# Kernel optimization log

Hardware: AMD Instinct MI355X
Metric: run time of the kernel (lower is better)

The kernel has to match this reference:

```python
import jax, jax.numpy as jnp
import numpy as np

NEG_SLOPE = 0.2  # PyG GATConv default negative_slope


def _gat_conv(x, src, dst, W, a_src, a_dst, bias, heads, concat):
    """PyG-style GATConv (eval mode, self-loops already appended to src/dst).
    x: [N, Fin], W: [Fin, heads*C], a_src/a_dst: [heads, C], bias matches output.
    """
    N = x.shape[0]
    C = W.shape[1] // heads
    xw = (x @ W).reshape(N, heads, C)                      # [N, H, C]
    alpha_s = jnp.sum(xw * a_src, axis=-1)                 # [N, H]
    alpha_d = jnp.sum(xw * a_dst, axis=-1)                 # [N, H]
    e = jax.nn.leaky_relu(alpha_s[src] + alpha_d[dst], NEG_SLOPE)  # [E, H]
    # softmax over incoming edges of each destination node (numerically stable)
    m = jax.ops.segment_max(e, dst, num_segments=N)        # [N, H]
    e = jnp.exp(e - m[dst])
    denom = jax.ops.segment_sum(e, dst, num_segments=N)    # [N, H]
    alpha = e / denom[dst]                                 # [E, H]
    out = jax.ops.segment_sum(alpha[:, :, None] * xw[src], dst, num_segments=N)  # [N, H, C]
    if concat:
        out = out.reshape(N, heads * C)
    else:
        out = out.mean(axis=1)
    return out + bias


def setup_inputs() -> dict:
    key = jax.random.key(0)
    ks = jax.random.split(key, 10)
    N, E, FIN, FOUT, H1, C1 = 100000, 1600000, 128, 16, 4, 8
    x = jax.random.normal(ks[0], (N, FIN), jnp.float32)
    edge_index = jax.random.randint(ks[1], (2, E), 0, N, dtype=jnp.int32)
    W1 = jax.random.normal(ks[2], (FIN, H1 * C1), jnp.float32) / np.sqrt(FIN)
    a1_src = jax.random.normal(ks[3], (H1, C1), jnp.float32) / np.sqrt(C1)
    a1_dst = jax.random.normal(ks[4], (H1, C1), jnp.float32) / np.sqrt(C1)
    b1 = jnp.zeros((H1 * C1,), jnp.float32)
    W2 = jax.random.normal(ks[5], (H1 * C1, FOUT), jnp.float32) / np.sqrt(H1 * C1)
    a2_src = jax.random.normal(ks[6], (1, FOUT), jnp.float32) / np.sqrt(FOUT)
    a2_dst = jax.random.normal(ks[7], (1, FOUT), jnp.float32) / np.sqrt(FOUT)
    b2 = jnp.zeros((FOUT,), jnp.float32)
    return {"x": x, "edge_index": edge_index, "W1": W1, "a1_src": a1_src,
            "a1_dst": a1_dst, "b1": b1, "W2": W2, "a2_src": a2_src,
            "a2_dst": a2_dst, "b2": b2}


def reference(x, edge_index, W1, a1_src, a1_dst, b1, W2, a2_src, a2_dst, b2):
    N = x.shape[0]
    # PyG GATConv add_self_loops=True default
    loop = jnp.arange(N, dtype=edge_index.dtype)
    src = jnp.concatenate([edge_index[0], loop])
    dst = jnp.concatenate([edge_index[1], loop])
    # eval mode: F.dropout is identity
    h = _gat_conv(x, src, dst, W1, a1_src, a1_dst, b1, heads=4, concat=True)
    h = jax.nn.elu(h)
    h = _gat_conv(h, src, dst, W2, a2_src, a2_dst, b2, heads=1, concat=True)
    return jax.nn.log_softmax(h, axis=1)
```

## Files before the change

### kernel.cpp

```cpp
#include <hip/hip_runtime.h>
#include <math.h>

#define NN 100000
#define NE 1600000
#define ET (NE + NN)
#define FIN 128
#define H1 4
#define C1 8
#define F1 32
#define FOUT 16
#define NSLOPE 0.2f

#define PARTW 256
#define PSHIFT 8
#define NPART ((NN + PARTW - 1) / PARTW)
#define CHUNK 8192
#define NBLK ((ET + CHUNK - 1) / CHUNK)
#define CPAD 16
#define SMASK 0x1FFFF

typedef _Float16 half8 __attribute__((ext_vector_type(8)));
typedef _Float16 half4_t __attribute__((ext_vector_type(4)));
typedef _Float16 half2_t __attribute__((ext_vector_type(2)));
typedef float f32x4 __attribute__((ext_vector_type(4)));

template <int SEL>
__device__ inline float fp8dec(unsigned int w) {
    return __builtin_amdgcn_cvt_f32_fp8((int)w, SEL);
}


__device__ inline int wave_incl_scan(int v) {
#pragma unroll
    for (int off = 1; off < 64; off <<= 1) {
        int u = __shfl_up(v, off);
        if ((threadIdx.x & 63) >= off) v += u;
    }
    return v;
}

__device__ inline int block_excl_scan(int v, int* wsum, int nw) {
    int t = threadIdx.x, wid = t >> 6, lane = t & 63;
    int incl = wave_incl_scan(v);
    if (lane == 63) wsum[wid] = incl;
    __syncthreads();
    if (wid == 0) {
        int wv = (lane < nw) ? wsum[lane] : 0;
        wv = wave_incl_scan(wv);
        if (lane < nw) wsum[lane] = wv;
    }
    __syncthreads();
    return incl - v + (wid ? wsum[wid - 1] : 0);
}


__global__ __launch_bounds__(1024) void k_hist(const int* __restrict__ dstA, int* __restrict__ ptotal) {
    __shared__ int h[NPART];
    int t = threadIdx.x;
    for (int i = t; i < NPART; i += 1024) h[i] = 0;
    __syncthreads();
    int base = blockIdx.x * CHUNK;
#pragma unroll
    for (int k = 0; k < CHUNK / 1024; k++) {
        int e = base + k * 1024 + t;
        if (e < ET) {
            int d = (e < NE) ? dstA[e] : (e - NE);
            atomicAdd(&h[d >> PSHIFT], 1);
        }
    }
    __syncthreads();
    for (int i = t; i < NPART; i += 1024)
        if (h[i]) atomicAdd(&ptotal[i * CPAD], h[i]);
}

__global__ __launch_bounds__(512) void k_pbase(const int* __restrict__ ptotal, int* __restrict__ pbase,
                                               int* __restrict__ gcur, int* __restrict__ rowstart) {
    __shared__ int wsum[8];
    int t = threadIdx.x;
    int v = (t < NPART) ? ptotal[t * CPAD] : 0;
    int excl = block_excl_scan(v, wsum, 8);
    if (t < NPART) { pbase[t] = excl; gcur[t * CPAD] = excl; }
    if (t == 0) { pbase[NPART] = ET; rowstart[NN] = ET; }
}

__global__ __launch_bounds__(1024) void k_part(const int* __restrict__ srcA, const int* __restrict__ dstA,
                                               int* __restrict__ gcur, int* __restrict__ pairs) {
    __shared__ int h[NPART];
    __shared__ int cur[NPART];
    int t = threadIdx.x;
    for (int i = t; i < NPART; i += 1024) h[i] = 0;
    __syncthreads();
    int base = blockIdx.x * CHUNK;
#pragma unroll
    for (int k = 0; k < CHUNK / 1024; k++) {
        int e = base + k * 1024 + t;
        if (e < ET) {
            int d = (e < NE) ? dstA[e] : (e - NE);
            atomicAdd(&h[d >> PSHIFT], 1);
        }
    }
    __syncthreads();
    for (int i = t; i < NPART; i += 1024) {
        int c = h[i];
        cur[i] = c ? atomicAdd(&gcur[i * CPAD], c) : 0;
    }
    __syncthreads();
#pragma unroll
    for (int k = 0; k < CHUNK / 1024; k++) {
        int e = base + k * 1024 + t;
        if (e < ET) {
            int s, d;
            if (e < NE) { s = srcA[e]; d = dstA[e]; }
            else        { s = e - NE;  d = s; }
            int pos = atomicAdd(&cur[d >> PSHIFT], 1);
            pairs[pos] = ((d & (PARTW - 1)) << 17) | s;
        }
    }
}

__global__ __launch_bounds__(1024) void k_sort(const int* __restrict__ pbase, const int* __restrict__ pairs,
                                               int* __restrict__ rowstart, int* __restrict__ epack) {
    __shared__ int hist[PARTW];
    __shared__ int sa[PARTW], sb[PARTW];
    int p = blockIdx.x;
    int t = threadIdx.x;
    int n0 = p << PSHIFT;
    int nn = min(PARTW, NN - n0);
    int base = pbase[p];
    int cnt = pbase[p + 1] - base;
    if (t < PARTW) hist[t] = 0;
    __syncthreads();
    for (int i = t; i < cnt; i += 1024)
        atomicAdd(&hist[pairs[base + i] >> 17], 1);
    __syncthreads();
    if (t < PARTW) sa[t] = hist[t];
    __syncthreads();
    int* pin = sa; int* pout = sb;
    for (int off = 1; off < PARTW; off <<= 1) {
        if (t < PARTW) pout[t] = pin[t] + ((t >= off) ? pin[t - off] : 0);
        __syncthreads();
        int* tmp = pin; pin = pout; pout = tmp;
    }
    int excl = 0;
    if (t < PARTW) {
        excl = pin[t] - hist[t];
        if (t < nn) rowstart[n0 + t] = base + excl;
    }
    __syncthreads();
    if (t < PARTW) hist[t] = excl;
    __syncthreads();
    for (int i = t; i < cnt; i += 1024) {
        int v = pairs[base + i];
        int pos = base + atomicAdd(&hist[v >> 17], 1);
        epack[pos] = v;
    }
}


__global__ __launch_bounds__(256) void k_gemm1(const float* __restrict__ x, const float* __restrict__ W1,
        const float* __restrict__ a1s, const float* __restrict__ a1d,
        unsigned int* __restrict__ xc1, float* __restrict__ ad1) {
    __shared__ _Float16 w1t[F1 * FIN];
    __shared__ float xs[256 * F1];
    int t = threadIdx.x;
    {
        int i0 = t * 16;
#pragma unroll
        for (int i = 0; i < 16; i++) {
            int idx = i0 + i;
            int k = idx >> 5, n = idx & 31;
            w1t[n * FIN + k] = (_Float16)W1[idx];
        }
    }
    __syncthreads();
    int w = t >> 6, l = t & 63;
    int q = l >> 4, r16 = l & 15;
    int nblk = blockIdx.x * 256;
    int n0 = nblk + w * 64;
    half8 bf[4][2];
#pragma unroll
    for (int kc = 0; kc < 4; kc++)
#pragma unroll
        for (int nt = 0; nt < 2; nt++)
            bf[kc][nt] = *(const half8*)&w1t[(nt * 16 + r16) * FIN + kc * 32 + q * 8];
#pragma unroll
    for (int mt = 0; mt < 4; mt++) {
        int row = n0 + mt * 16 + r16;
        int rowc = min(row, NN - 1);
        const float4* xp = (const float4*)(x + (size_t)rowc * FIN + q * 8);
        half8 af[4];
#pragma unroll
        for (int kc = 0; kc < 4; kc++) {
            float4 u = xp[kc * 8];
            float4 v = xp[kc * 8 + 1];
            half8 a;
            a[0] = (_Float16)u.x; a[1] = (_Float16)u.y; a[2] = (_Float16)u.z; a[3] = (_Float16)u.w;
            a[4] = (_Float16)v.x; a[5] = (_Float16)v.y; a[6] = (_Float16)v.z; a[7] = (_Float16)v.w;
            af[kc] = a;
        }
        f32x4 acc0 = {0.f, 0.f, 0.f, 0.f};
        f32x4 acc1 = {0.f, 0.f, 0.f, 0.f};
#pragma unroll
        for (int kc = 0; kc < 4; kc++) {
            acc0 = __builtin_amdgcn_mfma_f32_16x16x32_f16(af[kc], bf[kc][0], acc0, 0, 0, 0);
            acc1 = __builtin_amdgcn_mfma_f32_16x16x32_f16(af[kc], bf[kc][1], acc1, 0, 0, 0);
        }
#pragma unroll
        for (int r = 0; r < 4; r++) {
            xs[(w * 64 + mt * 16 + q * 4 + r) * F1 + r16] = acc0[r];
            xs[(w * 64 + mt * 16 + q * 4 + r) * F1 + 16 + r16] = acc1[r];
        }
    }
    int node = nblk + w * 64 + l;
    if (node < NN) {
        const float4* xr = (const float4*)&xs[(w * 64 + l) * F1];
        float rowv[F1];
#pragma unroll
        for (int j = 0; j < 8; j++) {
            float4 v = xr[j];
            rowv[j * 4] = v.x; rowv[j * 4 + 1] = v.y; rowv[j * 4 + 2] = v.z; rowv[j * 4 + 3] = v.w;
        }
        float ss[H1], dd[H1];
#pragma unroll
        for (int h = 0; h < H1; h++) {
            ss[h] = 0.f; dd[h] = 0.f;
#pragma unroll
            for (int c = 0; c < C1; c++) {
                ss[h] = fmaf(rowv[h * C1 + c], a1s[h * C1 + c], ss[h]);
                dd[h] = fmaf(rowv[h * C1 + c], a1d[h * C1 + c], dd[h]);
            }
        }
        uint4 o[4];
        unsigned int* ow = (unsigned int*)o;
#pragma unroll
        for (int c4 = 0; c4 < 8; c4++) {
            int p = 0;
            p = __builtin_amdgcn_cvt_pk_fp8_f32(rowv[c4 * 4 + 0], rowv[c4 * 4 + 1], p, false);
            p = __builtin_amdgcn_cvt_pk_fp8_f32(rowv[c4 * 4 + 2], rowv[c4 * 4 + 3], p, true);
            ow[2 * c4] = (unsigned int)p;
            ow[2 * c4 + 1] = __float_as_uint(ss[c4 >> 1]);
        }
        uint4* o16 = (uint4*)(xc1 + (size_t)node * 16);
        o16[0] = o[0];
        o16[1] = o[1];
        o16[2] = o[2];
        o16[3] = o[3];
        ((float4*)ad1)[node] = make_float4(dd[0], dd[1], dd[2], dd[3]);
    }
}


__global__ __launch_bounds__(256) void k_gather1(const int* __restrict__ rowstart, const int* __restrict__ epack,
        const float* __restrict__ ad1, const unsigned int* __restrict__ xc1,
        const float* __restrict__ b1, _Float16* __restrict__ h1h) {
    int n = blockIdx.x * 4 + (threadIdx.x >> 6);
    if (n >= NN) return;
    int l = threadIdx.x & 63;
    int g = l >> 3;
    int j = l & 7;
    int h = j >> 1;
    float adh = ad1[n * H1 + h];
    const uint2* xrow = (const uint2*)xc1;
    int beg = rowstart[n], end = rowstart[n + 1];
    float a0 = 0.f, a1 = 0.f, a2 = 0.f, a3 = 0.f, ad = 0.f;
    int i = beg + g;
    int c0 = epack[i] & SMASK, c1 = epack[i + 8] & SMASK;
    int sn0 = epack[i + 16] & SMASK, sn1 = epack[i + 24] & SMASK;
    uint2 t0 = xrow[c0 * 8 + j], t1 = xrow[c1 * 8 + j];
    unsigned int v0 = t0.x, v1 = t1.x;
    float f0 = __uint_as_float(t0.y), f1 = __uint_as_float(t1.y);
    while (i + 8 < end) {
        uint2 n0v = xrow[sn0 * 8 + j], n1v = xrow[sn1 * 8 + j];
        int u0 = epack[i + 32] & SMASK, u1 = epack[i + 40] & SMASK;
        float e0 = f0 + adh, e1 = f1 + adh;
        e0 = fmaxf(e0, NSLOPE * e0);
        e1 = fmaxf(e1, NSLOPE * e1);
        float w0 = __expf(e0), w1 = __expf(e1);
        ad += w0 + w1;
        a0 = fmaf(w0, fp8dec<0>(v0), fmaf(w1, fp8dec<0>(v1), a0));
        a1 = fmaf(w0, fp8dec<1>(v0), fmaf(w1, fp8dec<1>(v1), a1));
        a2 = fmaf(w0, fp8dec<2>(v0), fmaf(w1, fp8dec<2>(v1), a2));
        a3 = fmaf(w0, fp8dec<3>(v0), fmaf(w1, fp8dec<3>(v1), a3));
        v0 = n0v.x; v1 = n1v.x;
        f0 = __uint_as_float(n0v.y); f1 = __uint_as_float(n1v.y);
        sn0 = u0; sn1 = u1;
        i += 16;
    }
    if (i < end) {
        float e0 = f0 + adh;
        e0 = fmaxf(e0, NSLOPE * e0);
        float w0 = __expf(e0);
        ad += w0;
        a0 = fmaf(w0, fp8dec<0>(v0), a0);
        a1 = fmaf(w0, fp8dec<1>(v0), a1);
        a2 = fmaf(w0, fp8dec<2>(v0), a2);
        a3 = fmaf(w0, fp8dec<3>(v0), a3);
    }
#pragma unroll
    for (int off = 8; off < 64; off <<= 1) {
        a0 += __shfl_xor(a0, off);
        a1 += __shfl_xor(a1, off);
        a2 += __shfl_xor(a2, off);
        a3 += __shfl_xor(a3, off);
        ad += __shfl_xor(ad, off);
    }
    if (l < 8) {
        float inv = 1.0f / ad;
        float y0 = fmaf(a0, inv, b1[4 * j]);
        float y1 = fmaf(a1, inv, b1[4 * j + 1]);
        float y2 = fmaf(a2, inv, b1[4 * j + 2]);
        float y3 = fmaf(a3, inv, b1[4 * j + 3]);
        y0 = (y0 > 0.f) ? y0 : expm1f(y0);
        y1 = (y1 > 0.f) ? y1 : expm1f(y1);
        y2 = (y2 > 0.f) ? y2 : expm1f(y2);
        y3 = (y3 > 0.f) ? y3 : expm1f(y3);
        half4_t o;
        o[0] = (_Float16)y0; o[1] = (_Float16)y1; o[2] = (_Float16)y2; o[3] = (_Float16)y3;
        ((half4_t*)h1h)[(size_t)n * 8 + j] = o;
    }
}


__global__ __launch_bounds__(256) void k_node2(const _Float16* __restrict__ h1h, const float* __restrict__ W2,
        const float* __restrict__ a2s, const float* __restrict__ a2d,
        unsigned int* __restrict__ xc2, float* __restrict__ ad2) {
    int n = blockIdx.x * 256 + threadIdx.x;
    if (n >= NN) return;
    float acc[FOUT];
#pragma unroll
    for (int j = 0; j < FOUT; j++) acc[j] = 0.f;
    const half8* h8 = (const half8*)(h1h + (size_t)n * F1);
#pragma unroll
    for (int i8 = 0; i8 < F1 / 8; i8++) {
        half8 hv = h8[i8];
#pragma unroll
        for (int kk = 0; kk < 8; kk++) {
            float hk = (float)hv[kk];
            int i = i8 * 8 + kk;
#pragma unroll
            for (int j = 0; j < FOUT; j++)
                acc[j] = fmaf(hk, W2[i * FOUT + j], acc[j]);
        }
    }
    float ss = 0.f, dd = 0.f;
#pragma unroll
    for (int j = 0; j < FOUT; j++) {
        ss = fmaf(acc[j], a2s[j], ss);
        dd = fmaf(acc[j], a2d[j], dd);
    }
    uint4 o[4];
    unsigned int* ow = (unsigned int*)o;
    unsigned int ssu = __float_as_uint(ss);
#pragma unroll
    for (int p = 0; p < 8; p++) {
        half2_t hp;
        hp[0] = (_Float16)acc[2 * p];
        hp[1] = (_Float16)acc[2 * p + 1];
        ow[2 * p] = *(unsigned int*)&hp;
        ow[2 * p + 1] = ssu;
    }
    uint4* o16 = (uint4*)(xc2 + (size_t)n * 16);
    o16[0] = o[0];
    o16[1] = o[1];
    o16[2] = o[2];
    o16[3] = o[3];
    ad2[n] = dd;
}


__global__ __launch_bounds__(256) void k_gather2(const int* __restrict__ rowstart, const int* __restrict__ epack,
        const float* __restrict__ ad2, const unsigned int* __restrict__ xc2,
        const float* __restrict__ b2, float* __restrict__ out) {
    int n = blockIdx.x * 4 + (threadIdx.x >> 6);
    if (n >= NN) return;
    int l = threadIdx.x & 63;
    int g = l >> 3;
    int j = l & 7;
    float adn = ad2[n];
    const uint2* xrow = (const uint2*)xc2;
    int beg = rowstart[n], end = rowstart[n + 1];
    float a0 = 0.f, a1v = 0.f, ad = 0.f;
    int i = beg + g;
    int c0 = epack[i] & SMASK, c1 = epack[i + 8] & SMASK;
    int sn0 = epack[i + 16] & SMASK, sn1 = epack[i + 24] & SMASK;
    uint2 t0 = xrow[c0 * 8 + j], t1 = xrow[c1 * 8 + j];
    half2_t v0 = *(half2_t*)&t0.x, v1 = *(half2_t*)&t1.x;
    float f0 = __uint_as_float(t0.y), f1 = __uint_as_float(t1.y);
    while (i + 8 < end) {
        uint2 n0v = xrow[sn0 * 8 + j], n1v = xrow[sn1 * 8 + j];
        int u0 = epack[i + 32] & SMASK, u1 = epack[i + 40] & SMASK;
        float e0 = f0 + adn, e1 = f1 + adn;
        e0 = fmaxf(e0, NSLOPE * e0);
        e1 = fmaxf(e1, NSLOPE * e1);
        float w0 = __expf(e0), w1 = __expf(e1);
        ad += w0 + w1;
        a0  = fmaf(w0, (float)v0[0], fmaf(w1, (float)v1[0], a0));
        a1v = fmaf(w0, (float)v0[1], fmaf(w1, (float)v1[1], a1v));
        v0 = *(half2_t*)&n0v.x; v1 = *(half2_t*)&n1v.x;
        f0 = __uint_as_float(n0v.y); f1 = __uint_as_float(n1v.y);
        sn0 = u0; sn1 = u1;
        i += 16;
    }
    if (i < end) {
        float e0 = f0 + adn;
        e0 = fmaxf(e0, NSLOPE * e0);
        float w0 = __expf(e0);
        ad += w0;
        a0  = fmaf(w0, (float)v0[0], a0);
        a1v = fmaf(w0, (float)v0[1], a1v);
    }
#pragma unroll
    for (int off = 8; off < 64; off <<= 1) {
        a0  += __shfl_xor(a0, off);
        a1v += __shfl_xor(a1v, off);
        ad  += __shfl_xor(ad, off);
    }
    float inv = 1.0f / ad;
    float y0 = fmaf(a0, inv, b2[2 * j]);
    float y1 = fmaf(a1v, inv, b2[2 * j + 1]);
    float m = fmaxf(y0, y1);
#pragma unroll
    for (int off = 1; off < 8; off <<= 1) m = fmaxf(m, __shfl_xor(m, off));
    float s = __expf(y0 - m) + __expf(y1 - m);
#pragma unroll
    for (int off = 1; off < 8; off <<= 1) s += __shfl_xor(s, off);
    float ls = logf(s);
    if (l < 8)
        ((float2*)out)[(size_t)n * 8 + j] = make_float2(y0 - m - ls, y1 - m - ls);
}


extern "C" void kernel_launch(void* const* d_in, const int* in_sizes, int n_in,
                              void* d_out, int out_size, void* d_ws, size_t ws_size,
                              hipStream_t stream) {
    const float* x   = (const float*)d_in[0];
    const int*   ei  = (const int*)d_in[1];
    const float* W1  = (const float*)d_in[2];
    const float* a1s = (const float*)d_in[3];
    const float* a1d = (const float*)d_in[4];
    const float* b1  = (const float*)d_in[5];
    const float* W2  = (const float*)d_in[6];
    const float* a2s = (const float*)d_in[7];
    const float* a2d = (const float*)d_in[8];
    const float* b2  = (const float*)d_in[9];
    float* out = (float*)d_out;

    const int* srcA = ei;
    const int* dstA = ei + NE;

    char* w = (char*)d_ws;
    size_t off = 0;
    auto carve = [&](size_t bytes) -> void* {
        void* p = w + off;
        off = (off + bytes + 255) & ~(size_t)255;
        return p;
    };
    size_t xc1_off = off;
    unsigned int* xc1 = (unsigned int*)carve((size_t)NN * 64);
    float* ad1     = (float*)carve((size_t)NN * H1 * 4);
    _Float16* h1h  = (_Float16*)carve((size_t)NN * F1 * 2);
    unsigned int* xc2 = (unsigned int*)carve((size_t)NN * 64);
    float* ad2     = (float*)carve((size_t)NN * 4);
    int* pairs     = (int*)(w + xc1_off);
    int* rowstart  = (int*)carve((size_t)(NN + 1) * 4);
    int* epack     = (int*)carve((size_t)(ET + 64) * 4);
    int* ptotal    = (int*)carve((size_t)NPART * CPAD * 4);
    int* gcur      = (int*)carve((size_t)NPART * CPAD * 4);
    int* pbase     = (int*)carve((size_t)(NPART + 1) * 4);
    carve((size_t)2 * 1024 * 1024);
    (void)ws_size; (void)in_sizes; (void)n_in; (void)out_size;

    hipMemsetAsync(ptotal, 0, (size_t)NPART * CPAD * 4, stream);

    k_hist  <<<NBLK, 1024, 0, stream>>>(dstA, ptotal);
    k_pbase <<<1, 512, 0, stream>>>(ptotal, pbase, gcur, rowstart);
    k_part  <<<NBLK, 1024, 0, stream>>>(srcA, dstA, gcur, pairs);
    k_sort  <<<NPART, 1024, 0, stream>>>(pbase, pairs, rowstart, epack);

    k_gemm1 <<<(NN + 255) / 256, 256, 0, stream>>>(x, W1, a1s, a1d, xc1, ad1);
    k_gather1<<<(NN + 3) / 4, 256, 0, stream>>>(rowstart, epack, ad1, xc1, b1, h1h);
    k_node2 <<<(NN + 255) / 256, 256, 0, stream>>>(h1h, W2, a2s, a2d, xc2, ad2);
    k_gather2<<<(NN + 3) / 4, 256, 0, stream>>>(rowstart, epack, ad2, xc2, b2, out);
}
```

Before: 240.9 us.

## Split layer-1 gather table into two head halves, separate layer-2 score array

Result: slower. 282.4 us (+17.2%).

```diff
diff --git a/kernel.cpp b/kernel.cpp
--- a/kernel.cpp
+++ b/kernel.cpp
@@ -159,7 +159,8 @@
 
 __global__ __launch_bounds__(256) void k_gemm1(const float* __restrict__ x, const float* __restrict__ W1,
         const float* __restrict__ a1s, const float* __restrict__ a1d,
-        unsigned int* __restrict__ xc1, float* __restrict__ ad1) {
+        unsigned int* __restrict__ xcA, unsigned int* __restrict__ xcB,
+        float* __restrict__ ad1) {
     __shared__ _Float16 w1t[F1 * FIN];
     __shared__ float xs[256 * F1];
     int t = threadIdx.x;
@@ -220,6 +221,14 @@
             float4 v = xr[j];
             rowv[j * 4] = v.x; rowv[j * 4 + 1] = v.y; rowv[j * 4 + 2] = v.z; rowv[j * 4 + 3] = v.w;
         }
+        unsigned int fq[8];
+#pragma unroll
+        for (int c4 = 0; c4 < 8; c4++) {
+            int p = 0;
+            p = __builtin_amdgcn_cvt_pk_fp8_f32(rowv[c4 * 4 + 0], rowv[c4 * 4 + 1], p, false);
+            p = __builtin_amdgcn_cvt_pk_fp8_f32(rowv[c4 * 4 + 2], rowv[c4 * 4 + 3], p, true);
+            fq[c4] = (unsigned int)p;
+        }
         float ss[H1], dd[H1];
 #pragma unroll
         for (int h = 0; h < H1; h++) {
@@ -230,48 +239,43 @@
                 dd[h] = fmaf(rowv[h * C1 + c], a1d[h * C1 + c], dd[h]);
             }
         }
-        uint4 o[4];
-        unsigned int* ow = (unsigned int*)o;
-#pragma unroll
-        for (int c4 = 0; c4 < 8; c4++) {
-            int p = 0;
-            p = __builtin_amdgcn_cvt_pk_fp8_f32(rowv[c4 * 4 + 0], rowv[c4 * 4 + 1], p, false);
-            p = __builtin_amdgcn_cvt_pk_fp8_f32(rowv[c4 * 4 + 2], rowv[c4 * 4 + 3], p, true);
-            ow[2 * c4] = (unsigned int)p;
-            ow[2 * c4 + 1] = __float_as_uint(ss[c4 >> 1]);
-        }
-        uint4* o16 = (uint4*)(xc1 + (size_t)node * 16);
-        o16[0] = o[0];
-        o16[1] = o[1];
-        o16[2] = o[2];
-        o16[3] = o[3];
+        unsigned int s0 = __float_as_uint(ss[0]), s1 = __float_as_uint(ss[1]);
+        unsigned int s2 = __float_as_uint(ss[2]), s3 = __float_as_uint(ss[3]);
+        uint4* oa = (uint4*)(xcA + (size_t)node * 8);
+        oa[0] = make_uint4(fq[0], s0, fq[1], s0);
+        oa[1] = make_uint4(fq[2], s1, fq[3], s1);
+        uint4* ob = (uint4*)(xcB + (size_t)node * 8);
+        ob[0] = make_uint4(fq[4], s2, fq[5], s2);
+        ob[1] = make_uint4(fq[6], s3, fq[7], s3);
         ((float4*)ad1)[node] = make_float4(dd[0], dd[1], dd[2], dd[3]);
     }
 }
 
 
 __global__ __launch_bounds__(256) void k_gather1(const int* __restrict__ rowstart, const int* __restrict__ epack,
-        const float* __restrict__ ad1, const unsigned int* __restrict__ xc1,
+        const float* __restrict__ ad1, const unsigned int* __restrict__ xc,
         const float* __restrict__ b1, _Float16* __restrict__ h1h) {
     int n = blockIdx.x * 4 + (threadIdx.x >> 6);
     if (n >= NN) return;
     int l = threadIdx.x & 63;
-    int g = l >> 3;
-    int j = l & 7;
-    int h = j >> 1;
-    float adh = ad1[n * H1 + h];
-    const uint2* xrow = (const uint2*)xc1;
+    int g = l >> 2;
+    int j = l & 3;
+    float adh = ad1[n * H1 + (j >> 1)];
+    const uint2* xrow = (const uint2*)xc;
     int beg = rowstart[n], end = rowstart[n + 1];
     float a0 = 0.f, a1 = 0.f, a2 = 0.f, a3 = 0.f, ad = 0.f;
     int i = beg + g;
-    int c0 = epack[i] & SMASK, c1 = epack[i + 8] & SMASK;
-    int sn0 = epack[i + 16] & SMASK, sn1 = epack[i + 24] & SMASK;
-    uint2 t0 = xrow[c0 * 8 + j], t1 = xrow[c1 * 8 + j];
+    int c0 = __builtin_nontemporal_load(&epack[i]) & SMASK;
+    int c1 = __builtin_nontemporal_load(&epack[i + 16]) & SMASK;
+    int sn0 = __builtin_nontemporal_load(&epack[i + 32]) & SMASK;
+    int sn1 = __builtin_nontemporal_load(&epack[i + 48]) & SMASK;
+    uint2 t0 = xrow[c0 * 4 + j], t1 = xrow[c1 * 4 + j];
     unsigned int v0 = t0.x, v1 = t1.x;
     float f0 = __uint_as_float(t0.y), f1 = __uint_as_float(t1.y);
-    while (i + 8 < end) {
-        uint2 n0v = xrow[sn0 * 8 + j], n1v = xrow[sn1 * 8 + j];
-        int u0 = epack[i + 32] & SMASK, u1 = epack[i + 40] & SMASK;
+    while (i + 16 < end) {
+        uint2 n0v = xrow[sn0 * 4 + j], n1v = xrow[sn1 * 4 + j];
+        int u0 = __builtin_nontemporal_load(&epack[i + 64]) & SMASK;
+        int u1 = __builtin_nontemporal_load(&epack[i + 80]) & SMASK;
         float e0 = f0 + adh, e1 = f1 + adh;
         e0 = fmaxf(e0, NSLOPE * e0);
         e1 = fmaxf(e1, NSLOPE * e1);
@@ -284,7 +288,7 @@
         v0 = n0v.x; v1 = n1v.x;
         f0 = __uint_as_float(n0v.y); f1 = __uint_as_float(n1v.y);
         sn0 = u0; sn1 = u1;
-        i += 16;
+        i += 32;
     }
     if (i < end) {
         float e0 = f0 + adh;
@@ -297,14 +301,14 @@
         a3 = fmaf(w0, fp8dec<3>(v0), a3);
     }
 #pragma unroll
-    for (int off = 8; off < 64; off <<= 1) {
+    for (int off = 4; off < 64; off <<= 1) {
         a0 += __shfl_xor(a0, off);
         a1 += __shfl_xor(a1, off);
         a2 += __shfl_xor(a2, off);
         a3 += __shfl_xor(a3, off);
         ad += __shfl_xor(ad, off);
     }
-    if (l < 8) {
+    if (l < 4) {
         float inv = 1.0f / ad;
         float y0 = fmaf(a0, inv, b1[4 * j]);
         float y1 = fmaf(a1, inv, b1[4 * j + 1]);
@@ -316,14 +320,15 @@
         y3 = (y3 > 0.f) ? y3 : expm1f(y3);
         half4_t o;
         o[0] = (_Float16)y0; o[1] = (_Float16)y1; o[2] = (_Float16)y2; o[3] = (_Float16)y3;
-        ((half4_t*)h1h)[(size_t)n * 8 + j] = o;
+        __builtin_nontemporal_store(*(unsigned long long*)&o,
+            (unsigned long long*)(h1h + (size_t)n * F1 + 4 * j));
     }
 }
 
 
 __global__ __launch_bounds__(256) void k_node2(const _Float16* __restrict__ h1h, const float* __restrict__ W2,
         const float* __restrict__ a2s, const float* __restrict__ a2d,
-        unsigned int* __restrict__ xc2, float* __restrict__ ad2) {
+        unsigned int* __restrict__ xf2, float* __restrict__ as2f, float* __restrict__ ad2) {
     int n = blockIdx.x * 256 + threadIdx.x;
     if (n >= NN) return;
     float acc[FOUT];
@@ -348,47 +353,47 @@
         ss = fmaf(acc[j], a2s[j], ss);
         dd = fmaf(acc[j], a2d[j], dd);
     }
-    uint4 o[4];
+    uint4 o[2];
     unsigned int* ow = (unsigned int*)o;
-    unsigned int ssu = __float_as_uint(ss);
 #pragma unroll
     for (int p = 0; p < 8; p++) {
         half2_t hp;
         hp[0] = (_Float16)acc[2 * p];
         hp[1] = (_Float16)acc[2 * p + 1];
-        ow[2 * p] = *(unsigned int*)&hp;
-        ow[2 * p + 1] = ssu;
-    }
-    uint4* o16 = (uint4*)(xc2 + (size_t)n * 16);
+        ow[p] = *(unsigned int*)&hp;
+    }
+    uint4* o16 = (uint4*)(xf2 + (size_t)n * 8);
     o16[0] = o[0];
     o16[1] = o[1];
-    o16[2] = o[2];
-    o16[3] = o[3];
+    as2f[n] = ss;
     ad2[n] = dd;
 }
 
 
 __global__ __launch_bounds__(256) void k_gather2(const int* __restrict__ rowstart, const int* __restrict__ epack,
-        const float* __restrict__ ad2, const unsigned int* __restrict__ xc2,
-        const float* __restrict__ b2, float* __restrict__ out) {
+        const float* __restrict__ ad2, const unsigned int* __restrict__ xf2,
+        const float* __restrict__ as2f, const float* __restrict__ b2, float* __restrict__ out) {
     int n = blockIdx.x * 4 + (threadIdx.x >> 6);
     if (n >= NN) return;
     int l = threadIdx.x & 63;
     int g = l >> 3;
     int j = l & 7;
     float adn = ad2[n];
-    const uint2* xrow = (const uint2*)xc2;
+    const half2_t* xw = (const half2_t*)xf2;
     int beg = rowstart[n], end = rowstart[n + 1];
     float a0 = 0.f, a1v = 0.f, ad = 0.f;
     int i = beg + g;
-    int c0 = epack[i] & SMASK, c1 = epack[i + 8] & SMASK;
-    int sn0 = epack[i + 16] & SMASK, sn1 = epack[i + 24] & SMASK;
-    uint2 t0 = xrow[c0 * 8 + j], t1 = xrow[c1 * 8 + j];
-    half2_t v0 = *(half2_t*)&t0.x, v1 = *(half2_t*)&t1.x;
-    float f0 = __uint_as_float(t0.y), f1 = __uint_as_float(t1.y);
+    int c0 = __builtin_nontemporal_load(&epack[i]) & SMASK;
+    int c1 = __builtin_nontemporal_load(&epack[i + 8]) & SMASK;
+    int sn0 = __builtin_nontemporal_load(&epack[i + 16]) & SMASK;
+    int sn1 = __builtin_nontemporal_load(&epack[i + 24]) & SMASK;
+    float f0 = as2f[c0], f1 = as2f[c1];
+    half2_t v0 = xw[c0 * 8 + j], v1 = xw[c1 * 8 + j];
     while (i + 8 < end) {
-        uint2 n0v = xrow[sn0 * 8 + j], n1v = xrow[sn1 * 8 + j];
-        int u0 = epack[i + 32] & SMASK, u1 = epack[i + 40] & SMASK;
+        float nf0 = as2f[sn0], nf1 = as2f[sn1];
+        half2_t nv0 = xw[sn0 * 8 + j], nv1 = xw[sn1 * 8 + j];
+        int u0 = __builtin_nontemporal_load(&epack[i + 32]) & SMASK;
+        int u1 = __builtin_nontemporal_load(&epack[i + 40]) & SMASK;
         float e0 = f0 + adn, e1 = f1 + adn;
         e0 = fmaxf(e0, NSLOPE * e0);
         e1 = fmaxf(e1, NSLOPE * e1);
@@ -396,8 +401,8 @@
         ad += w0 + w1;
         a0  = fmaf(w0, (float)v0[0], fmaf(w1, (float)v1[0], a0));
         a1v = fmaf(w0, (float)v0[1], fmaf(w1, (float)v1[1], a1v));
-        v0 = *(half2_t*)&n0v.x; v1 = *(half2_t*)&n1v.x;
-        f0 = __uint_as_float(n0v.y); f1 = __uint_as_float(n1v.y);
+        v0 = nv0; v1 = nv1;
+        f0 = nf0; f1 = nf1;
         sn0 = u0; sn1 = u1;
         i += 16;
     }
@@ -425,8 +430,12 @@
 #pragma unroll
     for (int off = 1; off < 8; off <<= 1) s += __shfl_xor(s, off);
     float ls = logf(s);
-    if (l < 8)
-        ((float2*)out)[(size_t)n * 8 + j] = make_float2(y0 - m - ls, y1 - m - ls);
+    if (l < 8) {
+        float o0 = y0 - m - ls, o1 = y1 - m - ls;
+        unsigned long long u = ((unsigned long long)__float_as_uint(o1) << 32) | __float_as_uint(o0);
+        __builtin_nontemporal_store(u,
+            (unsigned long long*)&((float2*)out)[(size_t)n * 8 + j]);
+    }
 }
 
 
@@ -455,15 +464,17 @@
         off = (off + bytes + 255) & ~(size_t)255;
         return p;
     };
-    size_t xc1_off = off;
-    unsigned int* xc1 = (unsigned int*)carve((size_t)NN * 64);
+    size_t xc_off = off;
+    unsigned int* xcA = (unsigned int*)carve((size_t)NN * 32);
+    unsigned int* xcB = (unsigned int*)carve((size_t)NN * 32);
     float* ad1     = (float*)carve((size_t)NN * H1 * 4);
     _Float16* h1h  = (_Float16*)carve((size_t)NN * F1 * 2);
-    unsigned int* xc2 = (unsigned int*)carve((size_t)NN * 64);
+    unsigned int* xf2 = (unsigned int*)carve((size_t)NN * 32);
+    float* as2f    = (float*)carve((size_t)NN * 4);
     float* ad2     = (float*)carve((size_t)NN * 4);
-    int* pairs     = (int*)(w + xc1_off);
+    int* pairs     = (int*)(w + xc_off);
     int* rowstart  = (int*)carve((size_t)(NN + 1) * 4);
-    int* epack     = (int*)carve((size_t)(ET + 64) * 4);
+    int* epack     = (int*)carve((size_t)(ET + 128) * 4);
     int* ptotal    = (int*)carve((size_t)NPART * CPAD * 4);
     int* gcur      = (int*)carve((size_t)NPART * CPAD * 4);
     int* pbase     = (int*)carve((size_t)(NPART + 1) * 4);
@@ -477,8 +488,9 @@
     k_part  <<<NBLK, 1024, 0, stream>>>(srcA, dstA, gcur, pairs);
     k_sort  <<<NPART, 1024, 0, stream>>>(pbase, pairs, rowstart, epack);
 
-    k_gemm1 <<<(NN + 255) / 256, 256, 0, stream>>>(x, W1, a1s, a1d, xc1, ad1);
-    k_gather1<<<(NN + 3) / 4, 256, 0, stream>>>(rowstart, epack, ad1, xc1, b1, h1h);
-    k_node2 <<<(NN + 255) / 256, 256, 0, stream>>>(h1h, W2, a2s, a2d, xc2, ad2);
-    k_gather2<<<(NN + 3) / 4, 256, 0, stream>>>(rowstart, epack, ad2, xc2, b2, out);
-}
+    k_gemm1 <<<(NN + 255) / 256, 256, 0, stream>>>(x, W1, a1s, a1d, xcA, xcB, ad1);
+    k_gather1<<<(NN + 3) / 4, 256, 0, stream>>>(rowstart, epack, ad1,     xcA, b1,      h1h);
+    k_gather1<<<(NN + 3) / 4, 256, 0, stream>>>(rowstart, epack, ad1 + 2, xcB, b1 + 16, h1h + 16);
+    k_node2 <<<(NN + 255) / 256, 256, 0, stream>>>(h1h, W2, a2s, a2d, xf2, as2f, ad2);
+    k_gather2<<<(NN + 3) / 4, 256, 0, stream>>>(rowstart, epack, ad2, xf2, as2f, b2, out);
+}
```

## Replace CSR sort and per-node gather with partition-level LDS atomic accumulation

Applied to the files above, without the earlier changes.

Result: slower. 767.8 us (+218.8%).

```diff
diff --git a/kernel.cpp b/kernel.cpp
--- a/kernel.cpp
+++ b/kernel.cpp
@@ -11,22 +11,29 @@
 #define FOUT 16
 #define NSLOPE 0.2f
 
-#define PARTW 256
-#define PSHIFT 8
+#define PARTW 128
+#define PSHIFT 7
 #define NPART ((NN + PARTW - 1) / PARTW)
 #define CHUNK 8192
 #define NBLK ((ET + CHUNK - 1) / CHUNK)
 #define CPAD 16
 #define SMASK 0x1FFFF
 
+#define ASTRIDE 37
+#define A2STRIDE 17
+
 typedef _Float16 half8 __attribute__((ext_vector_type(8)));
-typedef _Float16 half4_t __attribute__((ext_vector_type(4)));
 typedef _Float16 half2_t __attribute__((ext_vector_type(2)));
 typedef float f32x4 __attribute__((ext_vector_type(4)));
 
 template <int SEL>
 __device__ inline float fp8dec(unsigned int w) {
     return __builtin_amdgcn_cvt_f32_fp8((int)w, SEL);
+}
+
+__device__ inline float lrelu_exp(float e) {
+    e = fmaxf(e, NSLOPE * e);
+    return __expf(e);
 }
 
 
@@ -73,14 +80,14 @@
         if (h[i]) atomicAdd(&ptotal[i * CPAD], h[i]);
 }
 
-__global__ __launch_bounds__(512) void k_pbase(const int* __restrict__ ptotal, int* __restrict__ pbase,
-                                               int* __restrict__ gcur, int* __restrict__ rowstart) {
-    __shared__ int wsum[8];
+__global__ __launch_bounds__(1024) void k_pbase(const int* __restrict__ ptotal, int* __restrict__ pbase,
+                                                int* __restrict__ gcur) {
+    __shared__ int wsum[16];
     int t = threadIdx.x;
     int v = (t < NPART) ? ptotal[t * CPAD] : 0;
-    int excl = block_excl_scan(v, wsum, 8);
+    int excl = block_excl_scan(v, wsum, 16);
     if (t < NPART) { pbase[t] = excl; gcur[t * CPAD] = excl; }
-    if (t == 0) { pbase[NPART] = ET; rowstart[NN] = ET; }
+    if (t == 0) pbase[NPART] = ET;
 }
 
 __global__ __launch_bounds__(1024) void k_part(const int* __restrict__ srcA, const int* __restrict__ dstA,
@@ -118,44 +125,6 @@
     }
 }
 
-__global__ __launch_bounds__(1024) void k_sort(const int* __restrict__ pbase, const int* __restrict__ pairs,
-                                               int* __restrict__ rowstart, int* __restrict__ epack) {
-    __shared__ int hist[PARTW];
-    __shared__ int sa[PARTW], sb[PARTW];
-    int p = blockIdx.x;
-    int t = threadIdx.x;
-    int n0 = p << PSHIFT;
-    int nn = min(PARTW, NN - n0);
-    int base = pbase[p];
-    int cnt = pbase[p + 1] - base;
-    if (t < PARTW) hist[t] = 0;
-    __syncthreads();
-    for (int i = t; i < cnt; i += 1024)
-        atomicAdd(&hist[pairs[base + i] >> 17], 1);
-    __syncthreads();
-    if (t < PARTW) sa[t] = hist[t];
-    __syncthreads();
-    int* pin = sa; int* pout = sb;
-    for (int off = 1; off < PARTW; off <<= 1) {
-        if (t < PARTW) pout[t] = pin[t] + ((t >= off) ? pin[t - off] : 0);
-        __syncthreads();
-        int* tmp = pin; pin = pout; pout = tmp;
-    }
-    int excl = 0;
-    if (t < PARTW) {
-        excl = pin[t] - hist[t];
-        if (t < nn) rowstart[n0 + t] = base + excl;
-    }
-    __syncthreads();
-    if (t < PARTW) hist[t] = excl;
-    __syncthreads();
-    for (int i = t; i < cnt; i += 1024) {
-        int v = pairs[base + i];
-        int pos = base + atomicAdd(&hist[v >> 17], 1);
-        epack[pos] = v;
-    }
-}
-
 
 __global__ __launch_bounds__(256) void k_gemm1(const float* __restrict__ x, const float* __restrict__ W1,
         const float* __restrict__ a1s, const float* __restrict__ a1d,
@@ -250,73 +219,107 @@
 }
 
 
-__global__ __launch_bounds__(256) void k_gather1(const int* __restrict__ rowstart, const int* __restrict__ epack,
+__global__ __launch_bounds__(256) void k_acc1(const int* __restrict__ pbase, const int* __restrict__ pairs,
         const float* __restrict__ ad1, const unsigned int* __restrict__ xc1,
         const float* __restrict__ b1, _Float16* __restrict__ h1h) {
-    int n = blockIdx.x * 4 + (threadIdx.x >> 6);
-    if (n >= NN) return;
-    int l = threadIdx.x & 63;
-    int g = l >> 3;
-    int j = l & 7;
-    int h = j >> 1;
-    float adh = ad1[n * H1 + h];
-    const uint2* xrow = (const uint2*)xc1;
-    int beg = rowstart[n], end = rowstart[n + 1];
-    float a0 = 0.f, a1 = 0.f, a2 = 0.f, a3 = 0.f, ad = 0.f;
-    int i = beg + g;
-    int c0 = epack[i] & SMASK, c1 = epack[i + 8] & SMASK;
-    int sn0 = epack[i + 16] & SMASK, sn1 = epack[i + 24] & SMASK;
-    uint2 t0 = xrow[c0 * 8 + j], t1 = xrow[c1 * 8 + j];
-    unsigned int v0 = t0.x, v1 = t1.x;
-    float f0 = __uint_as_float(t0.y), f1 = __uint_as_float(t1.y);
-    while (i + 8 < end) {
-        uint2 n0v = xrow[sn0 * 8 + j], n1v = xrow[sn1 * 8 + j];
-        int u0 = epack[i + 32] & SMASK, u1 = epack[i + 40] & SMASK;
-        float e0 = f0 + adh, e1 = f1 + adh;
-        e0 = fmaxf(e0, NSLOPE * e0);
-        e1 = fmaxf(e1, NSLOPE * e1);
-        float w0 = __expf(e0), w1 = __expf(e1);
-        ad += w0 + w1;
-        a0 = fmaf(w0, fp8dec<0>(v0), fmaf(w1, fp8dec<0>(v1), a0));
-        a1 = fmaf(w0, fp8dec<1>(v0), fmaf(w1, fp8dec<1>(v1), a1));
-        a2 = fmaf(w0, fp8dec<2>(v0), fmaf(w1, fp8dec<2>(v1), a2));
-        a3 = fmaf(w0, fp8dec<3>(v0), fmaf(w1, fp8dec<3>(v1), a3));
-        v0 = n0v.x; v1 = n1v.x;
-        f0 = __uint_as_float(n0v.y); f1 = __uint_as_float(n1v.y);
-        sn0 = u0; sn1 = u1;
-        i += 16;
-    }
-    if (i < end) {
-        float e0 = f0 + adh;
-        e0 = fmaxf(e0, NSLOPE * e0);
-        float w0 = __expf(e0);
-        ad += w0;
-        a0 = fmaf(w0, fp8dec<0>(v0), a0);
-        a1 = fmaf(w0, fp8dec<1>(v0), a1);
-        a2 = fmaf(w0, fp8dec<2>(v0), a2);
-        a3 = fmaf(w0, fp8dec<3>(v0), a3);
-    }
-#pragma unroll
-    for (int off = 8; off < 64; off <<= 1) {
-        a0 += __shfl_xor(a0, off);
-        a1 += __shfl_xor(a1, off);
-        a2 += __shfl_xor(a2, off);
-        a3 += __shfl_xor(a3, off);
-        ad += __shfl_xor(ad, off);
-    }
-    if (l < 8) {
-        float inv = 1.0f / ad;
-        float y0 = fmaf(a0, inv, b1[4 * j]);
-        float y1 = fmaf(a1, inv, b1[4 * j + 1]);
-        float y2 = fmaf(a2, inv, b1[4 * j + 2]);
-        float y3 = fmaf(a3, inv, b1[4 * j + 3]);
-        y0 = (y0 > 0.f) ? y0 : expm1f(y0);
-        y1 = (y1 > 0.f) ? y1 : expm1f(y1);
-        y2 = (y2 > 0.f) ? y2 : expm1f(y2);
-        y3 = (y3 > 0.f) ? y3 : expm1f(y3);
-        half4_t o;
-        o[0] = (_Float16)y0; o[1] = (_Float16)y1; o[2] = (_Float16)y2; o[3] = (_Float16)y3;
-        ((half4_t*)h1h)[(size_t)n * 8 + j] = o;
+    __shared__ float acc[PARTW * ASTRIDE];
+    __shared__ float adL[PARTW * H1];
+    int p = blockIdx.x, t = threadIdx.x;
+    int n0 = p << PSHIFT;
+    for (int i = t; i < PARTW * ASTRIDE; i += 256) acc[i] = 0.f;
+    for (int i = t; i < PARTW * H1; i += 256) {
+        int node = min(n0 + (i >> 2), NN - 1);
+        adL[i] = ad1[node * H1 + (i & 3)];
+    }
+    __syncthreads();
+    int base = pbase[p], cnt = pbase[p + 1] - base;
+    if (t < cnt) {
+        int v = pairs[base + t];
+        const uint4* rp = (const uint4*)(xc1 + (size_t)(v & SMASK) * 16);
+        uint4 r0 = rp[0], r1 = rp[1], r2 = rp[2], r3 = rp[3];
+        int i = t;
+        for (;;) {
+            int inext = i + 256;
+            bool more = inext < cnt;
+            int vn = 0;
+            uint4 q0 = make_uint4(0, 0, 0, 0), q1 = q0, q2 = q0, q3 = q0;
+            if (more) {
+                vn = pairs[base + inext];
+                const uint4* qp = (const uint4*)(xc1 + (size_t)(vn & SMASK) * 16);
+                q0 = qp[0]; q1 = qp[1]; q2 = qp[2]; q3 = qp[3];
+            }
+            int dloc = v >> 17;
+            float* ar = acc + dloc * ASTRIDE;
+            const float* al = adL + dloc * H1;
+            float w0 = lrelu_exp(__uint_as_float(r0.y) + al[0]);
+            float w1 = lrelu_exp(__uint_as_float(r1.y) + al[1]);
+            float w2 = lrelu_exp(__uint_as_float(r2.y) + al[2]);
+            float w3 = lrelu_exp(__uint_as_float(r3.y) + al[3]);
+            atomicAdd(&ar[32], w0);
+            atomicAdd(&ar[33], w1);
+            atomicAdd(&ar[34], w2);
+            atomicAdd(&ar[35], w3);
+            atomicAdd(&ar[0],  w0 * fp8dec<0>(r0.x));
+            atomicAdd(&ar[1],  w0 * fp8dec<1>(r0.x));
+            atomicAdd(&ar[2],  w0 * fp8dec<2>(r0.x));
+            atomicAdd(&ar[3],  w0 * fp8dec<3>(r0.x));
+            atomicAdd(&ar[4],  w0 * fp8dec<0>(r0.z));
+            atomicAdd(&ar[5],  w0 * fp8dec<1>(r0.z));
+            atomicAdd(&ar[6],  w0 * fp8dec<2>(r0.z));
+            atomicAdd(&ar[7],  w0 * fp8dec<3>(r0.z));
+            atomicAdd(&ar[8],  w1 * fp8dec<0>(r1.x));
+            atomicAdd(&ar[9],  w1 * fp8dec<1>(r1.x));
+            atomicAdd(&ar[10], w1 * fp8dec<2>(r1.x));
+            atomicAdd(&ar[11], w1 * fp8dec<3>(r1.x));
+            atomicAdd(&ar[12], w1 * fp8dec<0>(r1.z));
+            atomicAdd(&ar[13], w1 * fp8dec<1>(r1.z));
+            atomicAdd(&ar[14], w1 * fp8dec<2>(r1.z));
+            atomicAdd(&ar[15], w1 * fp8dec<3>(r1.z));
+            atomicAdd(&ar[16], w2 * fp8dec<0>(r2.x));
+            atomicAdd(&ar[17], w2 * fp8dec<1>(r2.x));
+            atomicAdd(&ar[18], w2 * fp8dec<2>(r2.x));
+            atomicAdd(&ar[19], w2 * fp8dec<3>(r2.x));
+            atomicAdd(&ar[20], w2 * fp8dec<0>(r2.z));
+            atomicAdd(&ar[21], w2 * fp8dec<1>(r2.z));
+            atomicAdd(&ar[22], w2 * fp8dec<2>(r2.z));
+            atomicAdd(&ar[23], w2 * fp8dec<3>(r2.z));
+            atomicAdd(&ar[24], w3 * fp8dec<0>(r3.x));
+            atomicAdd(&ar[25], w3 * fp8dec<1>(r3.x));
+            atomicAdd(&ar[26], w3 * fp8dec<2>(r3.x));
+            atomicAdd(&ar[27], w3 * fp8dec<3>(r3.x));
+            atomicAdd(&ar[28], w3 * fp8dec<0>(r3.z));
+            atomicAdd(&ar[29], w3 * fp8dec<1>(r3.z));
+            atomicAdd(&ar[30], w3 * fp8dec<2>(r3.z));
+            atomicAdd(&ar[31], w3 * fp8dec<3>(r3.z));
+            if (!more) break;
+            v = vn; r0 = q0; r1 = q1; r2 = q2; r3 = q3; i = inext;
+        }
+    }
+    __syncthreads();
+    int dloc = t >> 1, half = t & 1;
+    int n = n0 + dloc;
+    if (n < NN) {
+        float* ar = acc + dloc * ASTRIDE;
+        int c0 = half * 16;
+        int h0 = half * 2;
+        float invA = 1.0f / ar[32 + h0];
+        float invB = 1.0f / ar[33 + h0];
+        half8 o0, o1;
+#pragma unroll
+        for (int k = 0; k < 8; k++) {
+            float y = fmaf(ar[c0 + k], invA, b1[c0 + k]);
+            y = (y > 0.f) ? y : expm1f(y);
+            o0[k] = (_Float16)y;
+        }
+#pragma unroll
+        for (int k = 0; k < 8; k++) {
+            float y = fmaf(ar[c0 + 8 + k], invB, b1[c0 + 8 + k]);
+            y = (y > 0.f) ? y : expm1f(y);
+            o1[k] = (_Float16)y;
+        }
+        half8* dst = (half8*)(h1h + (size_t)n * F1 + c0);
+        dst[0] = o0;
+        dst[1] = o1;
     }
 }
 
@@ -368,65 +371,84 @@
 }
 
 
-__global__ __launch_bounds__(256) void k_gather2(const int* __restrict__ rowstart, const int* __restrict__ epack,
+__global__ __launch_bounds__(256) void k_acc2(const int* __restrict__ pbase, const int* __restrict__ pairs,
         const float* __restrict__ ad2, const unsigned int* __restrict__ xc2,
         const float* __restrict__ b2, float* __restrict__ out) {
-    int n = blockIdx.x * 4 + (threadIdx.x >> 6);
-    if (n >= NN) return;
-    int l = threadIdx.x & 63;
-    int g = l >> 3;
-    int j = l & 7;
-    float adn = ad2[n];
-    const uint2* xrow = (const uint2*)xc2;
-    int beg = rowstart[n], end = rowstart[n + 1];
-    float a0 = 0.f, a1v = 0.f, ad = 0.f;
-    int i = beg + g;
-    int c0 = epack[i] & SMASK, c1 = epack[i + 8] & SMASK;
-    int sn0 = epack[i + 16] & SMASK, sn1 = epack[i + 24] & SMASK;
-    uint2 t0 = xrow[c0 * 8 + j], t1 = xrow[c1 * 8 + j];
-    half2_t v0 = *(half2_t*)&t0.x, v1 = *(half2_t*)&t1.x;
-    float f0 = __uint_as_float(t0.y), f1 = __uint_as_float(t1.y);
-    while (i + 8 < end) {
-        uint2 n0v = xrow[sn0 * 8 + j], n1v = xrow[sn1 * 8 + j];
-        int u0 = epack[i + 32] & SMASK, u1 = epack[i + 40] & SMASK;
-        float e0 = f0 + adn, e1 = f1 + adn;
-        e0 = fmaxf(e0, NSLOPE * e0);
-        e1 = fmaxf(e1, NSLOPE * e1);
-        float w0 = __expf(e0), w1 = __expf(e1);
-        ad += w0 + w1;
-        a0  = fmaf(w0, (float)v0[0], fmaf(w1, (float)v1[0], a0));
-        a1v = fmaf(w0, (float)v0[1], fmaf(w1, (float)v1[1], a1v));
-        v0 = *(half2_t*)&n0v.x; v1 = *(half2_t*)&n1v.x;
-        f0 = __uint_as_float(n0v.y); f1 = __uint_as_float(n1v.y);
-        sn0 = u0; sn1 = u1;
-        i += 16;
-    }
-    if (i < end) {
-        float e0 = f0 + adn;
-        e0 = fmaxf(e0, NSLOPE * e0);
-        float w0 = __expf(e0);
-        ad += w0;
-        a0  = fmaf(w0, (float)v0[0], a0);
-        a1v = fmaf(w0, (float)v0[1], a1v);
-    }
-#pragma unroll
-    for (int off = 8; off < 64; off <<= 1) {
-        a0  += __shfl_xor(a0, off);
-        a1v += __shfl_xor(a1v, off);
-        ad  += __shfl_xor(ad, off);
-    }
-    float inv = 1.0f / ad;
-    float y0 = fmaf(a0, inv, b2[2 * j]);
-    float y1 = fmaf(a1v, inv, b2[2 * j + 1]);
-    float m = fmaxf(y0, y1);
-#pragma unroll
-    for (int off = 1; off < 8; off <<= 1) m = fmaxf(m, __shfl_xor(m, off));
-    float s = __expf(y0 - m) + __expf(y1 - m);
-#pragma unroll
-    for (int off = 1; off < 8; off <<= 1) s += __shfl_xor(s, off);
-    float ls = logf(s);
-    if (l < 8)
-        ((float2*)out)[(size_t)n * 8 + j] = make_float2(y0 - m - ls, y1 - m - ls);
+    __shared__ float acc[PARTW * A2STRIDE];
+    __shared__ float adL[PARTW];
+    int p = blockIdx.x, t = threadIdx.x;
+    int n0 = p << PSHIFT;
+    for (int i = t; i < PARTW * A2STRIDE; i += 256) acc[i] = 0.f;
+    if (t < PARTW) adL[t] = ad2[min(n0 + t, NN - 1)];
+    __syncthreads();
+    int base = pbase[p], cnt = pbase[p + 1] - base;
+    if (t < cnt) {
+        int v = pairs[base + t];
+        const uint4* rp = (const uint4*)(xc2 + (size_t)(v & SMASK) * 16);
+        uint4 r0 = rp[0], r1 = rp[1], r2 = rp[2], r3 = rp[3];
+        int i = t;
+        for (;;) {
+            int inext = i + 256;
+            bool more = inext < cnt;
+            int vn = 0;
+            uint4 q0 = make_uint4(0, 0, 0, 0), q1 = q0, q2 = q0, q3 = q0;
+            if (more) {
+                vn = pairs[base + inext];
+                const uint4* qp = (const uint4*)(xc2 + (size_t)(vn & SMASK) * 16);
+                q0 = qp[0]; q1 = qp[1]; q2 = qp[2]; q3 = qp[3];
+            }
+            int dloc = v >> 17;
+            float* ar = acc + dloc * A2STRIDE;
+            float w = lrelu_exp(__uint_as_float(r0.y) + adL[dloc]);
+            atomicAdd(&ar[16], w);
+            half2_t h0 = *(half2_t*)&r0.x, h1 = *(half2_t*)&r0.z;
+            half2_t h2 = *(half2_t*)&r1.x, h3 = *(half2_t*)&r1.z;
+            half2_t h4 = *(half2_t*)&r2.x, h5 = *(half2_t*)&r2.z;
+            half2_t h6 = *(half2_t*)&r3.x, h7 = *(half2_t*)&r3.z;
+            atomicAdd(&ar[0],  w * (float)h0[0]);
+            atomicAdd(&ar[1],  w * (float)h0[1]);
+            atomicAdd(&ar[2],  w * (float)h1[0]);
+            atomicAdd(&ar[3],  w * (float)h1[1]);
+            atomicAdd(&ar[4],  w * (float)h2[0]);
+            atomicAdd(&ar[5],  w * (float)h2[1]);
+            atomicAdd(&ar[6],  w * (float)h3[0]);
+            atomicAdd(&ar[7],  w * (float)h3[1]);
+            atomicAdd(&ar[8],  w * (float)h4[0]);
+            atomicAdd(&ar[9],  w * (float)h4[1]);
+            atomicAdd(&ar[10], w * (float)h5[0]);
+            atomicAdd(&ar[11], w * (float)h5[1]);
+            atomicAdd(&ar[12], w * (float)h6[0]);
+            atomicAdd(&ar[13], w * (float)h6[1]);
+            atomicAdd(&ar[14], w * (float)h7[0]);
+            atomicAdd(&ar[15], w * (float)h7[1]);
+            if (!more) break;
+            v = vn; r0 = q0; r1 = q1; r2 = q2; r3 = q3; i = inext;
+        }
+    }
+    __syncthreads();
+    if (t < PARTW) {
+        int n = n0 + t;
+        if (n < NN) {
+            float* ar = acc + t * A2STRIDE;
+            float inv = 1.0f / ar[16];
+            float y[FOUT];
+            float m = -1e30f;
+#pragma unroll
+            for (int c = 0; c < FOUT; c++) {
+                y[c] = fmaf(ar[c], inv, b2[c]);
+                m = fmaxf(m, y[c]);
+            }
+            float ssum = 0.f;
+#pragma unroll
+            for (int c = 0; c < FOUT; c++) ssum += __expf(y[c] - m);
+            float ls = m + logf(ssum);
+            float4* dst = (float4*)(out + (size_t)n * FOUT);
+#pragma unroll
+            for (int q = 0; q < 4; q++)
+                dst[q] = make_float4(y[4 * q] - ls, y[4 * q + 1] - ls,
+                                     y[4 * q + 2] - ls, y[4 * q + 3] - ls);
+        }
+    }
 }
 
 
@@ -455,30 +477,25 @@
         off = (off + bytes + 255) & ~(size_t)255;
         return p;
     };
-    size_t xc1_off = off;
     unsigned int* xc1 = (unsigned int*)carve((size_t)NN * 64);
     float* ad1     = (float*)carve((size_t)NN * H1 * 4);
     _Float16* h1h  = (_Float16*)carve((size_t)NN * F1 * 2);
     unsigned int* xc2 = (unsigned int*)carve((size_t)NN * 64);
     float* ad2     = (float*)carve((size_t)NN * 4);
-    int* pairs     = (int*)(w + xc1_off);
-    int* rowstart  = (int*)carve((size_t)(NN + 1) * 4);
-    int* epack     = (int*)carve((size_t)(ET + 64) * 4);
+    int* pairs     = (int*)carve((size_t)ET * 4);
     int* ptotal    = (int*)carve((size_t)NPART * CPAD * 4);
     int* gcur      = (int*)carve((size_t)NPART * CPAD * 4);
     int* pbase     = (int*)carve((size_t)(NPART + 1) * 4);
-    carve((size_t)2 * 1024 * 1024);
     (void)ws_size; (void)in_sizes; (void)n_in; (void)out_size;
 
     hipMemsetAsync(ptotal, 0, (size_t)NPART * CPAD * 4, stream);
 
     k_hist  <<<NBLK, 1024, 0, stream>>>(dstA, ptotal);
-    k_pbase <<<1, 512, 0, stream>>>(ptotal, pbase, gcur, rowstart);
+    k_pbase <<<1, 1024, 0, stream>>>(ptotal, pbase, gcur);
     k_part  <<<NBLK, 1024, 0, stream>>>(srcA, dstA, gcur, pairs);
-    k_sort  <<<NPART, 1024, 0, stream>>>(pbase, pairs, rowstart, epack);
 
     k_gemm1 <<<(NN + 255) / 256, 256, 0, stream>>>(x, W1, a1s, a1d, xc1, ad1);
-    k_gather1<<<(NN + 3) / 4, 256, 0, stream>>>(rowstart, epack, ad1, xc1, b1, h1h);
+    k_acc1  <<<NPART, 256, 0, stream>>>(pbase, pairs, ad1, xc1, b1, h1h);
     k_node2 <<<(NN + 255) / 256, 256, 0, stream>>>(h1h, W2, a2s, a2d, xc2, ad2);
-    k_gather2<<<(NN + 3) / 4, 256, 0, stream>>>(rowstart, epack, ad2, xc2, b2, out);
-}
+    k_acc2  <<<NPART, 256, 0, stream>>>(pbase, pairs, ad2, xc2, b2, out);
+}
```
